# Kernel optimization log

Hardware: AMD Instinct MI355X
Metric: run time of the kernel (lower is better)

Reference implementation:

```python
import jax, jax.numpy as jnp
import numpy as np

CHUNK = 128  # time_chunk_size from init_kwargs
EPS = 1e-8


def _forward(v, k, alpha, q):
    # v: (T,B,d), k/alpha/q: (T,B,n)
    T, B, d = v.shape
    n = k.shape[-1]
    nc = T // CHUNK  # T assumed divisible by CHUNK
    vr = v.reshape(nc, CHUNK, B, d)
    kr = k.reshape(nc, CHUNK, B, n)
    ar = alpha.reshape(nc, CHUNK, B, n)
    qr = q.reshape(nc, CHUNK, B, n)

    def step(S_prev, xs):
        vc, kc, ac, qc = xs  # (C,B,d), (C,B,n), ...
        outer = jnp.einsum('tbd,tbn->tbdn', vc, kc)          # (C,B,d,n)
        log_a = jnp.log(jnp.clip(ac, EPS))
        log_cp = jnp.cumsum(log_a, axis=0)                   # (C,B,n)
        cp = jnp.exp(log_cp)
        decay = cp / (cp[-1:] + EPS)                         # normalized per chunk
        S_local = jnp.cumsum(outer * decay[:, :, None, :], axis=0)
        prefix = jnp.exp(log_cp[0])                          # (B,n) decay of first step
        S_local = S_local + (S_prev * prefix[:, None, :])[None]
        y = jnp.einsum('tbdn,tbn->tbd', S_local, qc)         # (C,B,d)
        return S_local[-1], y

    S0 = jnp.zeros((B, d, n), v.dtype)
    _, ys = jax.lax.scan(step, S0, (vr, kr, ar, qr))
    return ys.reshape(T, B, d)


def setup_inputs() -> dict:
    key = jax.random.key(0)
    k1, k2, k3, k4 = jax.random.split(key, 4)
    T, B, d, n = 2048, 4, 256, 256
    return {
        'v': jax.random.normal(k1, (T, B, d), jnp.float32),
        'k': jax.random.normal(k2, (T, B, n), jnp.float32),
        'alpha': jax.random.uniform(k3, (T, B, n), jnp.float32),
        'q': jax.random.normal(k4, (T, B, n), jnp.float32),
    }


def reference(v, k, alpha, q):
    return _forward(v, k, alpha, q)
```

## Files before the change

kernel.cpp:

```cpp
#include <hip/hip_runtime.h>
#include <math.h>

typedef unsigned short u16;
typedef unsigned int u32;
typedef __bf16 bf16x8 __attribute__((ext_vector_type(8)));
typedef float f32x4 __attribute__((ext_vector_type(4)));

#define BB   4
#define DD   256
#define NN   256
#define CH   128
#define NCH  16
#define EPSF 1e-8f

#define WS_QB  0u
#define WS_VT  (4u<<20)
#define WS_WT  (8u<<20)
#define WS_WN  (12u<<20)
#define WS_AST (16u<<20)
#define WS_SPT (18u<<20)
#define WS_PF  (26u<<20)
#define WS_UT  (28u<<20)

__device__ __forceinline__ u16 f2bf(float x) {
  u32 u = __float_as_uint(x);
  u32 r = (u + 0x7fffu + ((u >> 16) & 1u)) >> 16;
  return (u16)r;
}
__device__ __forceinline__ float bf2f(u32 lo16) {
  return __uint_as_float(lo16 << 16);
}

__device__ __forceinline__ int xcd_swz(int bid, int nwg) {
  return (bid & 7) * (nwg >> 3) + (bid >> 3);
}

__device__ __forceinline__ void gload16(void* lds, const void* g) {
  __builtin_amdgcn_global_load_lds((const __attribute__((address_space(1))) void*)g,
                                   (__attribute__((address_space(3))) void*)lds, 16, 0, 0);
}

__device__ __forceinline__ void stage_tile(u16* lds, const u16* g, int rowstride) {
  int tid = threadIdx.x;
#pragma unroll
  for (int h = 0; h < 2; h++) {
    int ci = tid + h * 256;
    int r = ci >> 3, sl = ci & 7;
    const u16* src = g + (size_t)r * rowstride + ((sl ^ (r & 7)) << 3);
    gload16(lds + (size_t)ci * 8, src);
  }
}

__device__ __forceinline__ void stageA512(u16* lds, const u16* g, int rowstride) {
  int tid = threadIdx.x;
#pragma unroll
  for (int h = 0; h < 2; h++) {
    int ci = tid + h * 512;
    int r = ci >> 3, sl = ci & 7;
    const u16* src = g + (size_t)r * rowstride + ((sl ^ (r & 7)) << 3);
    gload16(lds + (size_t)ci * 8, src);
  }
}

__device__ __forceinline__ void stageB512(u16* lds, const u16* g, int rowstride) {
  int ci = threadIdx.x;
  int r = ci >> 3, sl = ci & 7;
  const u16* src = g + (size_t)r * rowstride + ((sl ^ (r & 7)) << 3);
  gload16(lds + (size_t)ci * 8, src);
}

__device__ __forceinline__ void read_frags(const u16* buf, int rbase, int lane,
                                           bf16x8 (&f)[2][2]) {
#pragma unroll
  for (int i = 0; i < 2; i++)
#pragma unroll
    for (int ks = 0; ks < 2; ks++) {
      int r = rbase + i * 16 + (lane & 15);
      int slot = ((ks << 2) + (lane >> 4)) ^ (r & 7);
      f[i][ks] = *reinterpret_cast<const bf16x8*>(buf + r * 64 + slot * 8);
    }
}

__device__ __forceinline__ void read_frags4(const u16* buf, int rbase, int lane,
                                            bf16x8 (&f)[4][2]) {
#pragma unroll
  for (int i = 0; i < 4; i++)
#pragma unroll
    for (int ks = 0; ks < 2; ks++) {
      int r = rbase + i * 16 + (lane & 15);
      int slot = ((ks << 2) + (lane >> 4)) ^ (r & 7);
      f[i][ks] = *reinterpret_cast<const bf16x8*>(buf + r * 64 + slot * 8);
    }
}

__device__ __forceinline__ void mma_step(const u16* Ab, const u16* Bb, int rm, int cn,
                                         int lane, f32x4 (&acc)[2][2]) {
  bf16x8 a[2][2], b[2][2];
  read_frags(Ab, rm, lane, a);
  read_frags(Bb, cn, lane, b);
#pragma unroll
  for (int mf = 0; mf < 2; mf++)
#pragma unroll
    for (int nf = 0; nf < 2; nf++)
#pragma unroll
      for (int ks = 0; ks < 2; ks++)
        acc[mf][nf] = __builtin_amdgcn_mfma_f32_16x16x32_bf16(a[mf][ks], b[nf][ks],
                                                              acc[mf][nf], 0, 0, 0);
}

__device__ __forceinline__ void mma_step8(const u16* Ab, const u16* Bb, int rm, int cn,
                                          int lane, f32x4 (&acc)[4][2]) {
  bf16x8 a[4][2], b[2][2];
  read_frags4(Ab, rm, lane, a);
  read_frags(Bb, cn, lane, b);
#pragma unroll
  for (int mf = 0; mf < 4; mf++)
#pragma unroll
    for (int nf = 0; nf < 2; nf++)
#pragma unroll
      for (int ks = 0; ks < 2; ks++)
        acc[mf][nf] = __builtin_amdgcn_mfma_f32_16x16x32_bf16(a[mf][ks], b[nf][ks],
                                                              acc[mf][nf], 0, 0, 0);
}

__global__ __launch_bounds__(256) void k_prep(const float* __restrict__ q,
                                              const float* __restrict__ v,
                                              const float* __restrict__ kin,
                                              const float* __restrict__ alpha,
                                              u16* __restrict__ qb,
                                              u16* __restrict__ vT,
                                              u16* __restrict__ wT,
                                              u16* __restrict__ wn,
                                              float* __restrict__ pf) {
  __shared__ __align__(16) char smem[64 * 136 * 2];
  int bid = blockIdx.x;
  int tid = threadIdx.x;
  if (bid < 256) {
    int ng = bid & 3, b = (bid >> 2) & 3, c = bid >> 4;
    int lane16 = tid & 15, seg = tid >> 4;
    int n0 = ng * 64 + lane16 * 4;
    int cb = c * BB + b;
    size_t gbase = ((size_t)(c * CH + seg * 8) * 1024) + b * NN + n0;

    float4 lg[8], kv[8];
    float4 a0 = {0.f, 0.f, 0.f, 0.f};
    float4 run = {0.f, 0.f, 0.f, 0.f};
#pragma unroll
    for (int i = 0; i < 8; i++) {
      float4 av = *(const float4*)&alpha[gbase + (size_t)i * 1024];
      av.x = fmaxf(av.x, EPSF); av.y = fmaxf(av.y, EPSF);
      av.z = fmaxf(av.z, EPSF); av.w = fmaxf(av.w, EPSF);
      kv[i] = *(const float4*)&kin[gbase + (size_t)i * 1024];
      if (i == 0) a0 = av;
      run.x += __logf(av.x); run.y += __logf(av.y);
      run.z += __logf(av.z); run.w += __logf(av.w);
      lg[i] = run;
    }

    float4 (*tot)[16] = (float4(*)[16])smem;
    tot[seg][lane16] = run;
    __syncthreads();
    float4 prefix = {0.f, 0.f, 0.f, 0.f}, total = {0.f, 0.f, 0.f, 0.f};
#pragma unroll
    for (int j = 0; j < 16; j++) {
      float4 tv = tot[j][lane16];
      if (j < seg) { prefix.x += tv.x; prefix.y += tv.y; prefix.z += tv.z; prefix.w += tv.w; }
      total.x += tv.x; total.y += tv.y; total.z += tv.z; total.w += tv.w;
    }
    float4 rden;
    rden.x = 1.f / (__expf(total.x) + EPSF);
    rden.y = 1.f / (__expf(total.y) + EPSF);
    rden.z = 1.f / (__expf(total.z) + EPSF);
    rden.w = 1.f / (__expf(total.w) + EPSF);

    union { u16 u[8]; uint4 v4; } pkn[4];
    u16* wncb = wn + (size_t)cb * (CH * NN);
#pragma unroll
    for (int i = 0; i < 8; i++) {
      union { u16 u[4]; uint2 v2; } row;
      row.u[0] = f2bf(kv[i].x * (__expf(prefix.x + lg[i].x) * rden.x));
      row.u[1] = f2bf(kv[i].y * (__expf(prefix.y + lg[i].y) * rden.y));
      row.u[2] = f2bf(kv[i].z * (__expf(prefix.z + lg[i].z) * rden.z));
      row.u[3] = f2bf(kv[i].w * (__expf(prefix.w + lg[i].w) * rden.w));
      pkn[0].u[i] = row.u[0]; pkn[1].u[i] = row.u[1];
      pkn[2].u[i] = row.u[2]; pkn[3].u[i] = row.u[3];
      *(uint2*)(wncb + (size_t)(seg * 8 + i) * NN + n0) = row.v2;
    }
    u16* wtcb = wT + (size_t)cb * (NN * CH);
#pragma unroll
    for (int j = 0; j < 4; j++)
      *(uint4*)(wtcb + (size_t)(n0 + j) * CH + seg * 8) = pkn[j].v4;
    if (seg == 0) *(float4*)&pf[cb * NN + n0] = a0;
  } else if (bid < 512) {
    int b2 = bid - 256;
    int dt = b2 & 3, cb = b2 >> 2;
    int c = cb >> 2, b = cb & 3;
    int d0 = dt * 64;
    u16* vt = (u16*)smem;
    int sr = tid >> 4, chd = tid & 15;
#pragma unroll
    for (int p = 0; p < 8; p++) {
      int s = p * 16 + sr;
      float4 x = *(const float4*)&v[((size_t)(c * CH + s) * BB + b) * DD + d0 + chd * 4];
      int dbase = chd * 4;
      vt[(dbase + 0) * 136 + s] = f2bf(x.x);
      vt[(dbase + 1) * 136 + s] = f2bf(x.y);
      vt[(dbase + 2) * 136 + s] = f2bf(x.z);
      vt[(dbase + 3) * 136 + s] = f2bf(x.w);
    }
    __syncthreads();
    int dr = tid >> 2, ch = tid & 3;
    const uint4* srcl = (const uint4*)&vt[dr * 136 + ch * 32];
    uint4 a0 = srcl[0], a1 = srcl[1], a2 = srcl[2], a3 = srcl[3];
    uint4* dst = (uint4*)&vT[((size_t)cb * DD + d0 + dr) * CH + ch * 32];
    dst[0] = a0; dst[1] = a1; dst[2] = a2; dst[3] = a3;
  } else {
    size_t gid = (size_t)(bid - 512) * 256 + tid;
    const float4* src = (const float4*)q + gid * 2;
    float4 x = src[0], z = src[1];
    union { u16 u[8]; uint4 v4; } pk;
    pk.u[0] = f2bf(x.x); pk.u[1] = f2bf(x.y); pk.u[2] = f2bf(x.z); pk.u[3] = f2bf(x.w);
    pk.u[4] = f2bf(z.x); pk.u[5] = f2bf(z.y); pk.u[6] = f2bf(z.z); pk.u[7] = f2bf(z.w);
    ((uint4*)qb)[gid] = pk.v4;
  }
}

__global__ __launch_bounds__(512) void k_ut(const u16* __restrict__ vT,
                                            const u16* __restrict__ wT,
                                            u16* __restrict__ utb) {
  __shared__ u16 Al[2][8192], Bl[2][8192];
  int bid = xcd_swz(blockIdx.x, 256);
  int tid = threadIdx.x, lane = tid & 63, wv = tid >> 6;
  int rm = (wv >> 2) * 64, cn = (wv & 3) * 32;
  int nt = bid & 1, dt = (bid >> 1) & 1, cb = bid >> 2;
  const u16* A = vT + ((size_t)cb * DD + dt * 128) * CH;
  const u16* B = wT + ((size_t)cb * NN + nt * 128) * CH;
  f32x4 acc[4][2] = {};
  stageA512(Al[0], A, CH);      stageA512(Al[1], A + 64, CH);
  stageA512(Bl[0], B, CH);      stageA512(Bl[1], B + 64, CH);
  __syncthreads();
  mma_step8(Al[0], Bl[0], rm, cn, lane, acc);
  mma_step8(Al[1], Bl[1], rm, cn, lane, acc);
  u16* out = utb + ((size_t)cb * DD + dt * 128) * NN + nt * 128;
#pragma unroll
  for (int mf = 0; mf < 4; mf++)
#pragma unroll
    for (int nf = 0; nf < 2; nf++)
#pragma unroll
      for (int r = 0; r < 4; r++) {
        int row = rm + mf * 16 + (lane >> 4) * 4 + r;
        int col = cn + nf * 16 + (lane & 15);
        out[(size_t)row * NN + col] = f2bf(acc[mf][nf][r]);
      }
}

__global__ __launch_bounds__(256) void k_scanas(const u16* __restrict__ qb,
                                                const u16* __restrict__ wn,
                                                const u32* __restrict__ utT2,
                                                const float* __restrict__ pf,
                                                u16* __restrict__ asT,
                                                u32* __restrict__ sptT2) {
  __shared__ u16 Al[2][4096], Bl[2][4096];
  int bid = blockIdx.x;
  int tid = threadIdx.x;
  if (bid < 192) {
    int lane = tid & 63, wv = tid >> 6;
    int rm = (wv >> 1) * 32, cn = (wv & 1) * 32;
    int tile = bid % 3;
    int cb = bid / 3;
    int ti = (tile == 0) ? 0 : 1;
    int si = (tile == 2) ? 1 : 0;
    int t0 = ti * 64, s0 = si * 64;
    int c = cb >> 2, b = cb & 3;
    const u16* A = qb + ((size_t)(c * CH + t0) * BB + b) * NN;
    const u16* B = wn + (size_t)cb * (CH * NN) + (size_t)s0 * NN;
    f32x4 acc[2][2] = {};
    stage_tile(Al[0], A, BB * NN); stage_tile(Bl[0], B, NN);
    __syncthreads();
    for (int st = 0; st < 4; st++) {
      int nx = st + 1;
      if (nx < 4) {
        stage_tile(Al[nx & 1], A + nx * 64, BB * NN);
        stage_tile(Bl[nx & 1], B + nx * 64, NN);
      }
      mma_step(Al[st & 1], Bl[st & 1], rm, cn, lane, acc);
      __syncthreads();
    }
    u16* outb = asT + (size_t)cb * (CH * CH);
#pragma unroll
    for (int mf = 0; mf < 2; mf++)
#pragma unroll
      for (int nf = 0; nf < 2; nf++)
#pragma unroll
        for (int r = 0; r < 4; r++) {
          int t = t0 + rm + mf * 16 + (lane >> 4) * 4 + r;
          int s = s0 + cn + nf * 16 + (lane & 15);
          float val = (s <= t) ? acc[mf][nf][r] : 0.f;
          outb[(size_t)t * CH + s] = f2bf(val);
        }
  } else {
    int id = (bid - 192) * 256 + tid;
    int nh = id & 127, dd = (id >> 7) & 255, b = id >> 15;
    u32 u[NCH];
    float2 pp[NCH];
#pragma unroll
    for (int ch = 0; ch < NCH; ch++) {
      int cb = ch * BB + b;
      u[ch] = utT2[((size_t)cb * DD + dd) * 128 + nh];
      pp[ch] = *(const float2*)&pf[cb * NN + nh * 2];
    }
    float S0 = 0.f, S1 = 0.f;
#pragma unroll
    for (int ch = 0; ch < NCH; ch++) {
      int cb = ch * BB + b;
      float Sp0 = S0 * pp[ch].x, Sp1 = S1 * pp[ch].y;
      sptT2[((size_t)cb * DD + dd) * 128 + nh] = (u32)f2bf(Sp0) | ((u32)f2bf(Sp1) << 16);
      S0 = Sp0 + bf2f(u[ch] & 0xffffu);
      S1 = Sp1 + bf2f(u[ch] >> 16);
    }
  }
}

__global__ __launch_bounds__(512) void k_out(const u16* __restrict__ qb,
                                             const u16* __restrict__ sptT,
                                             const u16* __restrict__ asT,
                                             const u16* __restrict__ vT,
                                             float* __restrict__ y) {
  int bid = xcd_swz(blockIdx.x, 256);
  int dt = bid & 3, cb = bid >> 2;
  int c = cb >> 2, b = cb & 3;
  int d0 = dt * 64;
  int tid = threadIdx.x, lane = tid & 63, wv = tid >> 6;
  int rm = (wv >> 1) * 32, cn = (wv & 1) * 32;
  const u16* A1 = qb + ((size_t)(c * CH) * BB + b) * NN;
  const u16* B1 = sptT + ((size_t)cb * DD + d0) * NN;
  const u16* A2 = asT + (size_t)cb * (CH * CH);
  const u16* B2 = vT + ((size_t)cb * DD + d0) * CH;
  __shared__ u16 Al[2][8192], Bl[2][4096];
  f32x4 acc[2][2] = {};

#define STG_OUT(s, bi)                                               \
  do {                                                               \
    if ((s) < 4) {                                                   \
      stageA512(Al[bi], A1 + (s) * 64, BB * NN);                     \
      stageB512(Bl[bi], B1 + (s) * 64, NN);                          \
    } else {                                                         \
      stageA512(Al[bi], A2 + ((s) - 4) * 64, CH);                    \
      stageB512(Bl[bi], B2 + ((s) - 4) * 64, CH);                    \
    }                                                                \
  } while (0)

  STG_OUT(0, 0);
  __syncthreads();
  for (int st = 0; st < 6; st++) {
    if (st + 1 < 6) STG_OUT(st + 1, (st + 1) & 1);
    if (st < 5 || rm >= 64)
      mma_step(Al[st & 1], Bl[st & 1], rm, cn, lane, acc);
    __syncthreads();
  }
#undef STG_OUT

  float* out = y + ((size_t)(c * CH) * BB + b) * DD + d0;
#pragma unroll
  for (int mf = 0; mf < 2; mf++)
#pragma unroll
    for (int nf = 0; nf < 2; nf++)
#pragma unroll
      for (int r = 0; r < 4; r++) {
        int row = rm + mf * 16 + (lane >> 4) * 4 + r;
        int col = cn + nf * 16 + (lane & 15);
        out[(size_t)row * (BB * DD) + col] = acc[mf][nf][r];
      }
}

extern "C" void kernel_launch(void* const* d_in, const int* in_sizes, int n_in,
                              void* d_out, int out_size, void* d_ws, size_t ws_size,
                              hipStream_t stream) {
  const float* v = (const float*)d_in[0];
  const float* k = (const float*)d_in[1];
  const float* alpha = (const float*)d_in[2];
  const float* q = (const float*)d_in[3];
  float* y = (float*)d_out;
  char* ws = (char*)d_ws;
  u16* qb = (u16*)(ws + WS_QB);
  u16* vT = (u16*)(ws + WS_VT);
  u16* wT = (u16*)(ws + WS_WT);
  u16* wn = (u16*)(ws + WS_WN);
  u16* asT = (u16*)(ws + WS_AST);
  u16* sptT = (u16*)(ws + WS_SPT);
  float* pf = (float*)(ws + WS_PF);
  u16* utb = (u16*)(ws + WS_UT);

  k_prep<<<1536, 256, 0, stream>>>(q, v, k, alpha, qb, vT, wT, wn, pf);
  k_ut<<<256, 512, 0, stream>>>(vT, wT, utb);
  k_scanas<<<704, 256, 0, stream>>>(qb, wn, (const u32*)utb, pf, asT, (u32*)sptT);
  k_out<<<256, 512, 0, stream>>>(qb, sptT, asT, vT, y);
}
```

Measured before the change: 34.39 us.

## Merge chunk-state GEMM with attention-score GEMM and fold scan into output kernel

The per-chunk state GEMM (U) now runs in the same launch as the intra-chunk score GEMM, using smaller 64x64 tiles over 1024 blocks. The inter-chunk state scan no longer has its own kernel and no longer writes a bf16 state buffer. Each output block instead recomputes the decayed prefix state for its rows directly from U and writes it into LDS as the B operand. This removes one launch and the round trip of the state buffer through global memory. In exchange, later chunks do redundant serial scan work that grows with the chunk index, which creates load imbalance and extra U reads.

```diff
diff --git a/kernel.cpp b/kernel.cpp
--- a/kernel.cpp
+++ b/kernel.cpp
@@ -18,7 +18,6 @@
 #define WS_WT  (8u<<20)
 #define WS_WN  (12u<<20)
 #define WS_AST (16u<<20)
-#define WS_SPT (18u<<20)
 #define WS_PF  (26u<<20)
 #define WS_UT  (28u<<20)
 
@@ -81,18 +80,6 @@
     }
 }
 
-__device__ __forceinline__ void read_frags4(const u16* buf, int rbase, int lane,
-                                            bf16x8 (&f)[4][2]) {
-#pragma unroll
-  for (int i = 0; i < 4; i++)
-#pragma unroll
-    for (int ks = 0; ks < 2; ks++) {
-      int r = rbase + i * 16 + (lane & 15);
-      int slot = ((ks << 2) + (lane >> 4)) ^ (r & 7);
-      f[i][ks] = *reinterpret_cast<const bf16x8*>(buf + r * 64 + slot * 8);
-    }
-}
-
 __device__ __forceinline__ void mma_step(const u16* Ab, const u16* Bb, int rm, int cn,
                                          int lane, f32x4 (&acc)[2][2]) {
   bf16x8 a[2][2], b[2][2];
@@ -100,21 +87,6 @@
   read_frags(Bb, cn, lane, b);
 #pragma unroll
   for (int mf = 0; mf < 2; mf++)
-#pragma unroll
-    for (int nf = 0; nf < 2; nf++)
-#pragma unroll
-      for (int ks = 0; ks < 2; ks++)
-        acc[mf][nf] = __builtin_amdgcn_mfma_f32_16x16x32_bf16(a[mf][ks], b[nf][ks],
-                                                              acc[mf][nf], 0, 0, 0);
-}
-
-__device__ __forceinline__ void mma_step8(const u16* Ab, const u16* Bb, int rm, int cn,
-                                          int lane, f32x4 (&acc)[4][2]) {
-  bf16x8 a[4][2], b[2][2];
-  read_frags4(Ab, rm, lane, a);
-  read_frags(Bb, cn, lane, b);
-#pragma unroll
-  for (int mf = 0; mf < 4; mf++)
 #pragma unroll
     for (int nf = 0; nf < 2; nf++)
 #pragma unroll
@@ -225,49 +197,19 @@
   }
 }
 
-__global__ __launch_bounds__(512) void k_ut(const u16* __restrict__ vT,
-                                            const u16* __restrict__ wT,
-                                            u16* __restrict__ utb) {
-  __shared__ u16 Al[2][8192], Bl[2][8192];
-  int bid = xcd_swz(blockIdx.x, 256);
+__global__ __launch_bounds__(256) void k_utas(const u16* __restrict__ vT,
+                                              const u16* __restrict__ wT,
+                                              const u16* __restrict__ qb,
+                                              const u16* __restrict__ wn,
+                                              u16* __restrict__ utb,
+                                              u16* __restrict__ asT) {
+  __shared__ u16 Al[2][4096], Bl[2][4096];
+  int bid0 = blockIdx.x;
   int tid = threadIdx.x, lane = tid & 63, wv = tid >> 6;
-  int rm = (wv >> 2) * 64, cn = (wv & 3) * 32;
-  int nt = bid & 1, dt = (bid >> 1) & 1, cb = bid >> 2;
-  const u16* A = vT + ((size_t)cb * DD + dt * 128) * CH;
-  const u16* B = wT + ((size_t)cb * NN + nt * 128) * CH;
-  f32x4 acc[4][2] = {};
-  stageA512(Al[0], A, CH);      stageA512(Al[1], A + 64, CH);
-  stageA512(Bl[0], B, CH);      stageA512(Bl[1], B + 64, CH);
-  __syncthreads();
-  mma_step8(Al[0], Bl[0], rm, cn, lane, acc);
-  mma_step8(Al[1], Bl[1], rm, cn, lane, acc);
-  u16* out = utb + ((size_t)cb * DD + dt * 128) * NN + nt * 128;
-#pragma unroll
-  for (int mf = 0; mf < 4; mf++)
-#pragma unroll
-    for (int nf = 0; nf < 2; nf++)
-#pragma unroll
-      for (int r = 0; r < 4; r++) {
-        int row = rm + mf * 16 + (lane >> 4) * 4 + r;
-        int col = cn + nf * 16 + (lane & 15);
-        out[(size_t)row * NN + col] = f2bf(acc[mf][nf][r]);
-      }
-}
-
-__global__ __launch_bounds__(256) void k_scanas(const u16* __restrict__ qb,
-                                                const u16* __restrict__ wn,
-                                                const u32* __restrict__ utT2,
-                                                const float* __restrict__ pf,
-                                                u16* __restrict__ asT,
-                                                u32* __restrict__ sptT2) {
-  __shared__ u16 Al[2][4096], Bl[2][4096];
-  int bid = blockIdx.x;
-  int tid = threadIdx.x;
-  if (bid < 192) {
-    int lane = tid & 63, wv = tid >> 6;
-    int rm = (wv >> 1) * 32, cn = (wv & 1) * 32;
-    int tile = bid % 3;
-    int cb = bid / 3;
+  int rm = (wv >> 1) * 32, cn = (wv & 1) * 32;
+  if (bid0 < 192) {
+    int tile = bid0 % 3;
+    int cb = bid0 / 3;
     int ti = (tile == 0) ? 0 : 1;
     int si = (tile == 2) ? 1 : 0;
     int t0 = ti * 64, s0 = si * 64;
@@ -299,33 +241,39 @@
           outb[(size_t)t * CH + s] = f2bf(val);
         }
   } else {
-    int id = (bid - 192) * 256 + tid;
-    int nh = id & 127, dd = (id >> 7) & 255, b = id >> 15;
-    u32 u[NCH];
-    float2 pp[NCH];
-#pragma unroll
-    for (int ch = 0; ch < NCH; ch++) {
-      int cb = ch * BB + b;
-      u[ch] = utT2[((size_t)cb * DD + dd) * 128 + nh];
-      pp[ch] = *(const float2*)&pf[cb * NN + nh * 2];
-    }
-    float S0 = 0.f, S1 = 0.f;
-#pragma unroll
-    for (int ch = 0; ch < NCH; ch++) {
-      int cb = ch * BB + b;
-      float Sp0 = S0 * pp[ch].x, Sp1 = S1 * pp[ch].y;
-      sptT2[((size_t)cb * DD + dd) * 128 + nh] = (u32)f2bf(Sp0) | ((u32)f2bf(Sp1) << 16);
-      S0 = Sp0 + bf2f(u[ch] & 0xffffu);
-      S1 = Sp1 + bf2f(u[ch] >> 16);
-    }
-  }
-}
-
-__global__ __launch_bounds__(512) void k_out(const u16* __restrict__ qb,
-                                             const u16* __restrict__ sptT,
-                                             const u16* __restrict__ asT,
-                                             const u16* __restrict__ vT,
-                                             float* __restrict__ y) {
+    int bid = xcd_swz(bid0 - 192, 1024);
+    int nt = bid & 3, dt = (bid >> 2) & 3, cb = bid >> 4;
+    const u16* A = vT + ((size_t)cb * DD + dt * 64) * CH;
+    const u16* B = wT + ((size_t)cb * NN + nt * 64) * CH;
+    f32x4 acc[2][2] = {};
+    stage_tile(Al[0], A, CH); stage_tile(Al[1], A + 64, CH);
+    stage_tile(Bl[0], B, CH); stage_tile(Bl[1], B + 64, CH);
+    __syncthreads();
+    mma_step(Al[0], Bl[0], rm, cn, lane, acc);
+    mma_step(Al[1], Bl[1], rm, cn, lane, acc);
+    u16* out = utb + ((size_t)cb * DD + dt * 64) * NN + nt * 64;
+#pragma unroll
+    for (int mf = 0; mf < 2; mf++)
+#pragma unroll
+      for (int nf = 0; nf < 2; nf++)
+#pragma unroll
+        for (int r = 0; r < 4; r++) {
+          int row = rm + mf * 16 + (lane >> 4) * 4 + r;
+          int col = cn + nf * 16 + (lane & 15);
+          out[(size_t)row * NN + col] = f2bf(acc[mf][nf][r]);
+        }
+  }
+}
+
+__global__ __launch_bounds__(512) void k_outscan(const u16* __restrict__ qb,
+                                                 const u16* __restrict__ asT,
+                                                 const u16* __restrict__ vT,
+                                                 const u16* __restrict__ utb,
+                                                 const float* __restrict__ pf,
+                                                 float* __restrict__ y) {
+  __shared__ u16 Al[2][8192];
+  __shared__ u16 Bl2[2][4096];
+  __shared__ u16 bspt[4][4096];
   int bid = xcd_swz(blockIdx.x, 256);
   int dt = bid & 3, cb = bid >> 2;
   int c = cb >> 2, b = cb & 3;
@@ -333,32 +281,62 @@
   int tid = threadIdx.x, lane = tid & 63, wv = tid >> 6;
   int rm = (wv >> 1) * 32, cn = (wv & 1) * 32;
   const u16* A1 = qb + ((size_t)(c * CH) * BB + b) * NN;
-  const u16* B1 = sptT + ((size_t)cb * DD + d0) * NN;
   const u16* A2 = asT + (size_t)cb * (CH * CH);
   const u16* B2 = vT + ((size_t)cb * DD + d0) * CH;
-  __shared__ u16 Al[2][8192], Bl[2][4096];
+
+  stageA512(Al[0], A1, BB * NN);
+
+  int row = tid >> 3;
+  int dr = d0 + row;
+  int n8 = (tid & 7) * 32;
+  float S[32];
+#pragma unroll
+  for (int j = 0; j < 32; j++) S[j] = 0.f;
+  for (int cp = 0; cp < c; cp++) {
+    int cbp = cp * BB + b;
+    const u32* urow = (const u32*)(utb + ((size_t)cbp * DD + dr) * NN + n8);
+    u32 ub[16];
+#pragma unroll
+    for (int j = 0; j < 16; j++) ub[j] = urow[j];
+#pragma unroll
+    for (int j = 0; j < 16; j++) {
+      float2 p = *(const float2*)&pf[cbp * NN + n8 + 2 * j];
+      S[2 * j]     = S[2 * j]     * p.x + bf2f(ub[j] & 0xffffu);
+      S[2 * j + 1] = S[2 * j + 1] * p.y + bf2f(ub[j] >> 16);
+    }
+  }
+  {
+    int cbc = c * BB + b;
+    int stg = (tid & 7) >> 1, half = tid & 1;
+#pragma unroll
+    for (int sl = 0; sl < 4; sl++) {
+      int col8 = half * 4 + sl;
+      int swsl = col8 ^ (row & 7);
+      union { u16 u[8]; uint4 v4; } pk;
+#pragma unroll
+      for (int e = 0; e < 8; e++) {
+        float p = pf[cbc * NN + n8 + sl * 8 + e];
+        pk.u[e] = f2bf(S[sl * 8 + e] * p);
+      }
+      *(uint4*)&bspt[stg][row * 64 + swsl * 8] = pk.v4;
+    }
+  }
+  __syncthreads();
+
   f32x4 acc[2][2] = {};
-
-#define STG_OUT(s, bi)                                               \
-  do {                                                               \
-    if ((s) < 4) {                                                   \
-      stageA512(Al[bi], A1 + (s) * 64, BB * NN);                     \
-      stageB512(Bl[bi], B1 + (s) * 64, NN);                          \
-    } else {                                                         \
-      stageA512(Al[bi], A2 + ((s) - 4) * 64, CH);                    \
-      stageB512(Bl[bi], B2 + ((s) - 4) * 64, CH);                    \
-    }                                                                \
-  } while (0)
-
-  STG_OUT(0, 0);
-  __syncthreads();
   for (int st = 0; st < 6; st++) {
-    if (st + 1 < 6) STG_OUT(st + 1, (st + 1) & 1);
+    int nx = st + 1;
+    if (nx < 4) {
+      stageA512(Al[nx & 1], A1 + nx * 64, BB * NN);
+    } else if (nx < 6) {
+      stageA512(Al[nx & 1], A2 + (nx - 4) * 64, CH);
+      stageB512(Bl2[nx & 1], B2 + (nx - 4) * 64, CH);
+    }
+    const u16* Bb = (st < 4) ? &bspt[st][0] : Bl2[st & 1];
     if (st < 5 || rm >= 64)
-      mma_step(Al[st & 1], Bl[st & 1], rm, cn, lane, acc);
-    __syncthreads();
-  }
-#undef STG_OUT
+      mma_step(Al[st & 1], Bb, rm, cn, lane, acc);
+    __syncthreads();
+  }
 
   float* out = y + ((size_t)(c * CH) * BB + b) * DD + d0;
 #pragma unroll
@@ -367,9 +345,9 @@
     for (int nf = 0; nf < 2; nf++)
 #pragma unroll
       for (int r = 0; r < 4; r++) {
-        int row = rm + mf * 16 + (lane >> 4) * 4 + r;
+        int orow = rm + mf * 16 + (lane >> 4) * 4 + r;
         int col = cn + nf * 16 + (lane & 15);
-        out[(size_t)row * (BB * DD) + col] = acc[mf][nf][r];
+        out[(size_t)orow * (BB * DD) + col] = acc[mf][nf][r];
       }
 }
 
@@ -387,12 +365,10 @@
   u16* wT = (u16*)(ws + WS_WT);
   u16* wn = (u16*)(ws + WS_WN);
   u16* asT = (u16*)(ws + WS_AST);
-  u16* sptT = (u16*)(ws + WS_SPT);
   float* pf = (float*)(ws + WS_PF);
   u16* utb = (u16*)(ws + WS_UT);
 
   k_prep<<<1536, 256, 0, stream>>>(q, v, k, alpha, qb, vT, wT, wn, pf);
-  k_ut<<<256, 512, 0, stream>>>(vT, wT, utb);
-  k_scanas<<<704, 256, 0, stream>>>(qb, wn, (const u32*)utb, pf, asT, (u32*)sptT);
-  k_out<<<256, 512, 0, stream>>>(qb, sptT, asT, vT, y);
-}
+  k_utas<<<1216, 256, 0, stream>>>(vT, wT, qb, wn, utb, asT);
+  k_outscan<<<256, 512, 0, stream>>>(qb, asT, vT, utb, pf, y);
+}
```

After: 61.82 us. 79.8% more time.
